# Performance work log

Measured on AMD Instinct MI355X. Metric: run time of the kernel, lower is better.

Reference implementation:

```python
import jax, jax.numpy as jnp
import numpy as np

N, K, T = 100000, 12, 365
PERIODS = (0.25, 0.5, 1.0, 2.0)
TWO_PI = 2.0 * np.pi


def _smooth_amplitude(param, idx, w, sf):
    # param: [N], idx: [N,K], w: [N,K]
    neigh = param[idx]                                   # gather [N,K]
    wavg = jnp.sum(neigh * w, axis=1)                    # [N]
    var = jnp.var(neigh, axis=1, ddof=1)                 # torch.var unbiased
    af = sf / (1.0 + var * 0.1)
    return (1.0 - af) * param + af * wavg


def _smooth_phase(param, idx, w, sf):
    cur_re, cur_im = jnp.cos(param), jnp.sin(param)      # unit complex, split re/im
    neigh = param[idx]                                   # [N,K]
    wav_re = jnp.sum(jnp.cos(neigh) * w, axis=1)
    wav_im = jnp.sum(jnp.sin(neigh) * w, axis=1)
    consistency = jnp.sqrt(wav_re * wav_re + wav_im * wav_im)
    af = sf * consistency
    mix_re = (1.0 - af) * cur_re + af * wav_re
    mix_im = (1.0 - af) * cur_im + af * wav_im
    return jnp.arctan2(mix_im, mix_re)                   # torch.angle


def setup_inputs() -> dict:
    key = jax.random.key(0)
    ks = jax.random.split(key, 6)
    time_vector = (jnp.arange(T, dtype=jnp.float32) / 365.25)
    constant_offset = jax.random.normal(ks[0], (N,), dtype=jnp.float32)
    linear_trend = jax.random.normal(ks[1], (N,), dtype=jnp.float32)  # ps00_rates buffer
    seasonal_amplitudes = jax.random.uniform(ks[2], (N, 4), dtype=jnp.float32) * 4.0
    seasonal_phases = jax.random.uniform(ks[3], (N, 4), dtype=jnp.float32) * TWO_PI
    neighbor_indices = jax.random.randint(ks[4], (N, K), 0, N, dtype=jnp.int32)
    w = jax.random.uniform(ks[5], (N, K), dtype=jnp.float32) + 1e-3
    neighbor_weights = w / jnp.sum(w, axis=1, keepdims=True)  # row-normalized like _compute_enhanced_weights
    return {
        'time_vector': time_vector,
        'constant_offset': constant_offset,
        'linear_trend': linear_trend,
        'seasonal_amplitudes': seasonal_amplitudes,
        'seasonal_phases': seasonal_phases,
        'neighbor_weights': neighbor_weights,
        'neighbor_indices': neighbor_indices,
    }


def reference(time_vector, constant_offset, linear_trend, seasonal_amplitudes,
              seasonal_phases, neighbor_weights, neighbor_indices):
    t = time_vector[None, :]                              # [1,T]
    signals = constant_offset[:, None] + linear_trend[:, None] * t  # [N,T]
    for i, period in enumerate(PERIODS):
        amp = _smooth_amplitude(seasonal_amplitudes[:, i], neighbor_indices,
                                neighbor_weights, 0.25)
        ph = _smooth_phase(seasonal_phases[:, i], neighbor_indices,
                           neighbor_weights, 0.15)
        freq = 1.0 / period
        signals = signals + amp[:, None] * jnp.sin(TWO_PI * freq * t + ph[:, None])
    return signals
```

## Files before the change

### kernel.cpp

```cpp
#include <hip/hip_runtime.h>

#define N_PTS 100000
#define KNB   12
#define TLEN  365
#define FUSED_ROWS 64
#define SYNTH_ROWS 16
#define PARAMS_BYTES ((size_t)N_PTS * 12 * sizeof(float))


__device__ __forceinline__ float bf2f(unsigned short u) {
    return __uint_as_float(((unsigned int)u) << 16);
}
__device__ __forceinline__ unsigned short f2bf(float f) {
    unsigned int x = __float_as_uint(f);
    unsigned int r = (x + 0x7FFFu + ((x >> 16) & 1u)) >> 16;
    return (unsigned short)r;
}

__device__ __forceinline__ bool detect_bf16(const void* tvec) {
    return ((const unsigned int*)tvec)[0] != 0u;
}

__device__ __forceinline__ float ld(const void* p, size_t i, bool b16) {
    if (b16) return bf2f(((const unsigned short*)p)[i]);
    return ((const float*)p)[i];
}

__device__ void compute_params(
    int n, bool b16,
    const void* __restrict__ amps,
    const void* __restrict__ phs,
    const void* __restrict__ wgts,
    const int*  __restrict__ idx,
    const void* __restrict__ coff,
    const void* __restrict__ trend,
    float outp[12])
{
    float sx[4]  = {0,0,0,0}, sxx[4] = {0,0,0,0}, swx[4] = {0,0,0,0};
    float wre[4] = {0,0,0,0}, wim[4] = {0,0,0,0};

    #pragma unroll
    for (int k = 0; k < KNB; ++k) {
        int j = idx[(size_t)n * KNB + k];
        j = (j < 0) ? 0 : ((j >= N_PTS) ? N_PTS - 1 : j);
        float wk = ld(wgts, (size_t)n * KNB + k, b16);
        #pragma unroll
        for (int i = 0; i < 4; ++i) {
            float a = ld(amps, (size_t)j * 4 + i, b16);
            float p = ld(phs,  (size_t)j * 4 + i, b16);
            sx[i]  += a;
            sxx[i] += a * a;
            swx[i] += wk * a;
            float s, c;
            __sincosf(p, &s, &c);
            wre[i] += wk * c;
            wim[i] += wk * s;
        }
    }

    outp[0] = ld(coff,  n, b16);
    outp[1] = ld(trend, n, b16);
    #pragma unroll
    for (int i = 0; i < 4; ++i) {
        float aof = ld(amps, (size_t)n * 4 + i, b16);
        float pof = ld(phs,  (size_t)n * 4 + i, b16);

        float mean  = sx[i] * (1.0f / KNB);
        float var   = fmaxf((sxx[i] - (float)KNB * mean * mean) * (1.0f / (KNB - 1)), 0.0f);
        float afa   = 0.25f / (1.0f + 0.1f * var);
        float amp_s = (1.0f - afa) * aof + afa * swx[i];

        float cons = sqrtf(wre[i] * wre[i] + wim[i] * wim[i]);
        float afp  = 0.15f * cons;
        float s, c;
        __sincosf(pof, &s, &c);
        float mre = (1.0f - afp) * c + afp * wre[i];
        float mim = (1.0f - afp) * s + afp * wim[i];
        float h   = sqrtf(mre * mre + mim * mim);
        float ai, bi;
        if (h > 1e-30f) {
            float scale = amp_s / h;
            ai = mre * scale;
            bi = mim * scale;
        } else {
            ai = amp_s;
            bi = 0.0f;
        }
        outp[2 + i] = ai;
        outp[6 + i] = bi;
    }
}

__device__ __forceinline__ void synth_row_store(
    void* out, size_t o, float v, bool b16)
{
    if (b16) ((unsigned short*)out)[o] = f2bf(v);
    else     ((float*)out)[o] = v;
}


#define NCOL 6

__global__ __launch_bounds__(64) void fused64_kernel(
    const void* __restrict__ amps,
    const void* __restrict__ phs,
    const void* __restrict__ wgts,
    const int*  __restrict__ idx,
    const void* __restrict__ coff,
    const void* __restrict__ trend,
    const void* __restrict__ tvec,
    void*       __restrict__ out)
{
    __shared__ float P[FUSED_ROWS][12];
    bool b16 = detect_bf16(tvec);

    int row0 = blockIdx.x * FUSED_ROWS;
    int tid  = threadIdx.x;

    int n = row0 + tid;
    if (n < N_PTS) {
        float outp[12];
        compute_params(n, b16, amps, phs, wgts, idx, coff, trend, outp);
        #pragma unroll
        for (int i = 0; i < 12; ++i) P[tid][i] = outp[i];
    }
    __syncthreads();

    const float W0 = 25.132741228718345f;
    const float W1 = 12.566370614359172f;
    const float W2 = 6.283185307179586f;
    const float W3 = 3.141592653589793f;

    float tv[NCOL];
    float s0[NCOL], c0[NCOL], s1[NCOL], c1[NCOL];
    float s2[NCOL], c2[NCOL], s3[NCOL], c3[NCOL];
    #pragma unroll
    for (int c = 0; c < NCOL; ++c) {
        int t = tid + 64 * c;
        float tval = (t < TLEN) ? ld(tvec, t, b16) : 0.0f;
        tv[c] = tval;
        __sincosf(W0 * tval, &s0[c], &c0[c]);
        __sincosf(W1 * tval, &s1[c], &c1[c]);
        __sincosf(W2 * tval, &s2[c], &c2[c]);
        __sincosf(W3 * tval, &s3[c], &c3[c]);
    }

    int rend = min(row0 + FUSED_ROWS, N_PTS) - row0;
    for (int r = 0; r < rend; ++r) {
        float p0 = P[r][0], p1 = P[r][1];
        float p2 = P[r][2], p3 = P[r][3], p4 = P[r][4], p5 = P[r][5];
        float p6 = P[r][6], p7 = P[r][7], p8 = P[r][8], p9 = P[r][9];
        size_t base = (size_t)(row0 + r) * TLEN;
        #pragma unroll
        for (int c = 0; c < NCOL; ++c) {
            int t = tid + 64 * c;
            if (t < TLEN) {
                float v = fmaf(p1, tv[c], p0);
                v = fmaf(p2, s0[c], v);
                v = fmaf(p3, s1[c], v);
                v = fmaf(p4, s2[c], v);
                v = fmaf(p5, s3[c], v);
                v = fmaf(p6, c0[c], v);
                v = fmaf(p7, c1[c], v);
                v = fmaf(p8, c2[c], v);
                v = fmaf(p9, c3[c], v);
                synth_row_store(out, base + t, v, b16);
            }
        }
    }
}


__global__ __launch_bounds__(256) void smooth_kernel(
    const void* __restrict__ amps,
    const void* __restrict__ phs,
    const void* __restrict__ wgts,
    const int*  __restrict__ idx,
    const void* __restrict__ coff,
    const void* __restrict__ trend,
    const void* __restrict__ tvec,
    float*      __restrict__ params)
{
    int n = blockIdx.x * blockDim.x + threadIdx.x;
    if (n >= N_PTS) return;
    bool b16 = detect_bf16(tvec);
    float outp[12];
    compute_params(n, b16, amps, phs, wgts, idx, coff, trend, outp);
    #pragma unroll
    for (int i = 0; i < 12; ++i) params[(size_t)n * 12 + i] = outp[i];
}

__global__ __launch_bounds__(384) void synth_kernel(
    const float* __restrict__ params,
    const void*  __restrict__ tvec,
    void*        __restrict__ out)
{
    bool b16 = detect_bf16(tvec);
    int t = threadIdx.x;
    if (t >= TLEN) return;
    float tval = ld(tvec, t, b16);

    const float W0 = 25.132741228718345f;
    const float W1 = 12.566370614359172f;
    const float W2 = 6.283185307179586f;
    const float W3 = 3.141592653589793f;
    float s0, c0, s1, c1, s2, c2, s3, c3;
    __sincosf(W0 * tval, &s0, &c0);
    __sincosf(W1 * tval, &s1, &c1);
    __sincosf(W2 * tval, &s2, &c2);
    __sincosf(W3 * tval, &s3, &c3);

    int row0 = blockIdx.x * SYNTH_ROWS;
    int rend = min(row0 + SYNTH_ROWS, N_PTS);
    for (int n = row0; n < rend; ++n) {
        const float* p = params + (size_t)n * 12;
        float v = fmaf(p[1], tval, p[0]);
        v = fmaf(p[2], s0, v);
        v = fmaf(p[3], s1, v);
        v = fmaf(p[4], s2, v);
        v = fmaf(p[5], s3, v);
        v = fmaf(p[6], c0, v);
        v = fmaf(p[7], c1, v);
        v = fmaf(p[8], c2, v);
        v = fmaf(p[9], c3, v);
        synth_row_store(out, (size_t)n * TLEN + t, v, b16);
    }
}

extern "C" void kernel_launch(void* const* d_in, const int* in_sizes, int n_in,
                              void* d_out, int out_size, void* d_ws, size_t ws_size,
                              hipStream_t stream) {
    const void* tvec  = d_in[0];
    const void* coff  = d_in[1];
    const void* trend = d_in[2];
    const void* amps  = d_in[3];
    const void* phs   = d_in[4];
    const void* wgts  = d_in[5];
    const int*  idx   = (const int*)d_in[6];

    int fblk = (N_PTS + FUSED_ROWS - 1) / FUSED_ROWS;
    fused64_kernel<<<fblk, 64, 0, stream>>>(
        amps, phs, wgts, idx, coff, trend, tvec, d_out);
}
```

Baseline: 223.5 us.

## Shrink rows per block to 16, broadcast params via readlane, vectorize gathers

Each 64-thread block now handles 16 rows instead of 64. Only the first 16 lanes compute the smoothed parameters, and each row's coefficients are broadcast to the wave with readlane instead of going through shared memory with a barrier. Index, weight and neighbour amplitude/phase loads use int4/float4 vector loads in the fp32 path. This gives four times as many blocks, which shortens the serial per-block synthesis loop and should balance the load better. The cost is that 48 lanes sit idle during the gather phase, and the per-block sincos precompute of the time basis is repeated four times as often.

Result: faster. 194.2 us (-13.1%).

```diff
diff --git a/kernel.cpp b/kernel.cpp
--- a/kernel.cpp
+++ b/kernel.cpp
@@ -3,9 +3,8 @@
 #define N_PTS 100000
 #define KNB   12
 #define TLEN  365
-#define FUSED_ROWS 64
-#define SYNTH_ROWS 16
-#define PARAMS_BYTES ((size_t)N_PTS * 12 * sizeof(float))
+#define ROWS  16
+#define NCOL  6
 
 
 __device__ __forceinline__ float bf2f(unsigned short u) {
@@ -24,6 +23,10 @@
 __device__ __forceinline__ float ld(const void* p, size_t i, bool b16) {
     if (b16) return bf2f(((const unsigned short*)p)[i]);
     return ((const float*)p)[i];
+}
+
+__device__ __forceinline__ float rl(float v, int lane) {
+    return __int_as_float(__builtin_amdgcn_readlane(__float_as_int(v), lane));
 }
 
 __device__ void compute_params(
@@ -39,31 +42,80 @@
     float sx[4]  = {0,0,0,0}, sxx[4] = {0,0,0,0}, swx[4] = {0,0,0,0};
     float wre[4] = {0,0,0,0}, wim[4] = {0,0,0,0};
 
+    int jj[KNB];
+    {
+        const int4* i4 = (const int4*)(idx + (size_t)n * KNB);
+        #pragma unroll
+        for (int q = 0; q < 3; ++q) {
+            int4 v = i4[q];
+            jj[q*4+0] = v.x; jj[q*4+1] = v.y; jj[q*4+2] = v.z; jj[q*4+3] = v.w;
+        }
+    }
+    float wk[KNB];
+    if (!b16) {
+        const float4* w4 = (const float4*)((const float*)wgts + (size_t)n * KNB);
+        #pragma unroll
+        for (int q = 0; q < 3; ++q) {
+            float4 v = w4[q];
+            wk[q*4+0] = v.x; wk[q*4+1] = v.y; wk[q*4+2] = v.z; wk[q*4+3] = v.w;
+        }
+    } else {
+        #pragma unroll
+        for (int k = 0; k < KNB; ++k) wk[k] = ld(wgts, (size_t)n * KNB + k, true);
+    }
+
     #pragma unroll
     for (int k = 0; k < KNB; ++k) {
-        int j = idx[(size_t)n * KNB + k];
+        int j = jj[k];
         j = (j < 0) ? 0 : ((j >= N_PTS) ? N_PTS - 1 : j);
-        float wk = ld(wgts, (size_t)n * KNB + k, b16);
+        float wkk = wk[k];
+        float av[4], pv[4];
+        if (!b16) {
+            float4 a4 = *(const float4*)((const float*)amps + (size_t)j * 4);
+            float4 p4 = *(const float4*)((const float*)phs  + (size_t)j * 4);
+            av[0] = a4.x; av[1] = a4.y; av[2] = a4.z; av[3] = a4.w;
+            pv[0] = p4.x; pv[1] = p4.y; pv[2] = p4.z; pv[3] = p4.w;
+        } else {
+            #pragma unroll
+            for (int i = 0; i < 4; ++i) {
+                av[i] = ld(amps, (size_t)j * 4 + i, true);
+                pv[i] = ld(phs,  (size_t)j * 4 + i, true);
+            }
+        }
         #pragma unroll
         for (int i = 0; i < 4; ++i) {
-            float a = ld(amps, (size_t)j * 4 + i, b16);
-            float p = ld(phs,  (size_t)j * 4 + i, b16);
+            float a = av[i], p = pv[i];
             sx[i]  += a;
             sxx[i] += a * a;
-            swx[i] += wk * a;
+            swx[i] += wkk * a;
             float s, c;
             __sincosf(p, &s, &c);
-            wre[i] += wk * c;
-            wim[i] += wk * s;
+            wre[i] += wkk * c;
+            wim[i] += wkk * s;
         }
     }
 
     outp[0] = ld(coff,  n, b16);
     outp[1] = ld(trend, n, b16);
+
+    float aof4[4], pof4[4];
+    if (!b16) {
+        float4 a4 = *(const float4*)((const float*)amps + (size_t)n * 4);
+        float4 p4 = *(const float4*)((const float*)phs  + (size_t)n * 4);
+        aof4[0] = a4.x; aof4[1] = a4.y; aof4[2] = a4.z; aof4[3] = a4.w;
+        pof4[0] = p4.x; pof4[1] = p4.y; pof4[2] = p4.z; pof4[3] = p4.w;
+    } else {
+        #pragma unroll
+        for (int i = 0; i < 4; ++i) {
+            aof4[i] = ld(amps, (size_t)n * 4 + i, true);
+            pof4[i] = ld(phs,  (size_t)n * 4 + i, true);
+        }
+    }
+
     #pragma unroll
     for (int i = 0; i < 4; ++i) {
-        float aof = ld(amps, (size_t)n * 4 + i, b16);
-        float pof = ld(phs,  (size_t)n * 4 + i, b16);
+        float aof = aof4[i];
+        float pof = pof4[i];
 
         float mean  = sx[i] * (1.0f / KNB);
         float var   = fmaxf((sxx[i] - (float)KNB * mean * mean) * (1.0f / (KNB - 1)), 0.0f);
@@ -99,9 +151,7 @@
 }
 
 
-#define NCOL 6
-
-__global__ __launch_bounds__(64) void fused64_kernel(
+__global__ __launch_bounds__(64, 1) void fused_r16_kernel(
     const void* __restrict__ amps,
     const void* __restrict__ phs,
     const void* __restrict__ wgts,
@@ -111,20 +161,15 @@
     const void* __restrict__ tvec,
     void*       __restrict__ out)
 {
-    __shared__ float P[FUSED_ROWS][12];
     bool b16 = detect_bf16(tvec);
-
-    int row0 = blockIdx.x * FUSED_ROWS;
     int tid  = threadIdx.x;
-
+    int row0 = blockIdx.x * ROWS;
+
+    float outp[12] = {0,0,0,0,0,0,0,0,0,0,0,0};
     int n = row0 + tid;
-    if (n < N_PTS) {
-        float outp[12];
+    if (tid < ROWS && n < N_PTS) {
         compute_params(n, b16, amps, phs, wgts, idx, coff, trend, outp);
-        #pragma unroll
-        for (int i = 0; i < 12; ++i) P[tid][i] = outp[i];
-    }
-    __syncthreads();
+    }
 
     const float W0 = 25.132741228718345f;
     const float W1 = 12.566370614359172f;
@@ -135,95 +180,45 @@
     float s0[NCOL], c0[NCOL], s1[NCOL], c1[NCOL];
     float s2[NCOL], c2[NCOL], s3[NCOL], c3[NCOL];
     #pragma unroll
-    for (int c = 0; c < NCOL; ++c) {
-        int t = tid + 64 * c;
+    for (int cc = 0; cc < NCOL; ++cc) {
+        int t = tid + 64 * cc;
         float tval = (t < TLEN) ? ld(tvec, t, b16) : 0.0f;
-        tv[c] = tval;
-        __sincosf(W0 * tval, &s0[c], &c0[c]);
-        __sincosf(W1 * tval, &s1[c], &c1[c]);
-        __sincosf(W2 * tval, &s2[c], &c2[c]);
-        __sincosf(W3 * tval, &s3[c], &c3[c]);
-    }
-
-    int rend = min(row0 + FUSED_ROWS, N_PTS) - row0;
+        tv[cc] = tval;
+        __sincosf(W0 * tval, &s0[cc], &c0[cc]);
+        __sincosf(W1 * tval, &s1[cc], &c1[cc]);
+        __sincosf(W2 * tval, &s2[cc], &c2[cc]);
+        __sincosf(W3 * tval, &s3[cc], &c3[cc]);
+    }
+
+    int rend = min(row0 + ROWS, N_PTS) - row0;
     for (int r = 0; r < rend; ++r) {
-        float p0 = P[r][0], p1 = P[r][1];
-        float p2 = P[r][2], p3 = P[r][3], p4 = P[r][4], p5 = P[r][5];
-        float p6 = P[r][6], p7 = P[r][7], p8 = P[r][8], p9 = P[r][9];
+        float p0 = rl(outp[0], r);
+        float p1 = rl(outp[1], r);
+        float p2 = rl(outp[2], r);
+        float p3 = rl(outp[3], r);
+        float p4 = rl(outp[4], r);
+        float p5 = rl(outp[5], r);
+        float p6 = rl(outp[6], r);
+        float p7 = rl(outp[7], r);
+        float p8 = rl(outp[8], r);
+        float p9 = rl(outp[9], r);
         size_t base = (size_t)(row0 + r) * TLEN;
         #pragma unroll
-        for (int c = 0; c < NCOL; ++c) {
-            int t = tid + 64 * c;
+        for (int cc = 0; cc < NCOL; ++cc) {
+            int t = tid + 64 * cc;
             if (t < TLEN) {
-                float v = fmaf(p1, tv[c], p0);
-                v = fmaf(p2, s0[c], v);
-                v = fmaf(p3, s1[c], v);
-                v = fmaf(p4, s2[c], v);
-                v = fmaf(p5, s3[c], v);
-                v = fmaf(p6, c0[c], v);
-                v = fmaf(p7, c1[c], v);
-                v = fmaf(p8, c2[c], v);
-                v = fmaf(p9, c3[c], v);
+                float v = fmaf(p1, tv[cc], p0);
+                v = fmaf(p2, s0[cc], v);
+                v = fmaf(p3, s1[cc], v);
+                v = fmaf(p4, s2[cc], v);
+                v = fmaf(p5, s3[cc], v);
+                v = fmaf(p6, c0[cc], v);
+                v = fmaf(p7, c1[cc], v);
+                v = fmaf(p8, c2[cc], v);
+                v = fmaf(p9, c3[cc], v);
                 synth_row_store(out, base + t, v, b16);
             }
         }
-    }
-}
-
-
-__global__ __launch_bounds__(256) void smooth_kernel(
-    const void* __restrict__ amps,
-    const void* __restrict__ phs,
-    const void* __restrict__ wgts,
-    const int*  __restrict__ idx,
-    const void* __restrict__ coff,
-    const void* __restrict__ trend,
-    const void* __restrict__ tvec,
-    float*      __restrict__ params)
-{
-    int n = blockIdx.x * blockDim.x + threadIdx.x;
-    if (n >= N_PTS) return;
-    bool b16 = detect_bf16(tvec);
-    float outp[12];
-    compute_params(n, b16, amps, phs, wgts, idx, coff, trend, outp);
-    #pragma unroll
-    for (int i = 0; i < 12; ++i) params[(size_t)n * 12 + i] = outp[i];
-}
-
-__global__ __launch_bounds__(384) void synth_kernel(
-    const float* __restrict__ params,
-    const void*  __restrict__ tvec,
-    void*        __restrict__ out)
-{
-    bool b16 = detect_bf16(tvec);
-    int t = threadIdx.x;
-    if (t >= TLEN) return;
-    float tval = ld(tvec, t, b16);
-
-    const float W0 = 25.132741228718345f;
-    const float W1 = 12.566370614359172f;
-    const float W2 = 6.283185307179586f;
-    const float W3 = 3.141592653589793f;
-    float s0, c0, s1, c1, s2, c2, s3, c3;
-    __sincosf(W0 * tval, &s0, &c0);
-    __sincosf(W1 * tval, &s1, &c1);
-    __sincosf(W2 * tval, &s2, &c2);
-    __sincosf(W3 * tval, &s3, &c3);
-
-    int row0 = blockIdx.x * SYNTH_ROWS;
-    int rend = min(row0 + SYNTH_ROWS, N_PTS);
-    for (int n = row0; n < rend; ++n) {
-        const float* p = params + (size_t)n * 12;
-        float v = fmaf(p[1], tval, p[0]);
-        v = fmaf(p[2], s0, v);
-        v = fmaf(p[3], s1, v);
-        v = fmaf(p[4], s2, v);
-        v = fmaf(p[5], s3, v);
-        v = fmaf(p[6], c0, v);
-        v = fmaf(p[7], c1, v);
-        v = fmaf(p[8], c2, v);
-        v = fmaf(p[9], c3, v);
-        synth_row_store(out, (size_t)n * TLEN + t, v, b16);
     }
 }
 
@@ -238,7 +233,7 @@
     const void* wgts  = d_in[5];
     const int*  idx   = (const int*)d_in[6];
 
-    int fblk = (N_PTS + FUSED_ROWS - 1) / FUSED_ROWS;
-    fused64_kernel<<<fblk, 64, 0, stream>>>(
+    int fblk = (N_PTS + ROWS - 1) / ROWS;
+    fused_r16_kernel<<<fblk, 64, 0, stream>>>(
         amps, phs, wgts, idx, coff, trend, tvec, d_out);
 }
```
